# Kernel optimization log

Measured on AMD Instinct MI355X. Metric: run time of the kernel, lower is better.

## Reference

```python
import jax, jax.numpy as jnp
import numpy as np

S, IN, OUT = 2048, 512, 512
H, KV = 16, 4            # query heads, kv heads (cross-broadcast + averaged)
DQ = DK = DV = 64        # per-head embedding dims


def setup_inputs() -> dict:
    key = jax.random.key(0)
    ks = jax.random.split(key, 5)
    lim_in = 1.0 / np.sqrt(IN)
    lim_o = 1.0 / np.sqrt(H * DV)
    x = jax.random.normal(ks[0], (S, IN), dtype=jnp.float32)
    Wq = jax.random.uniform(ks[1], (H * DQ, IN), jnp.float32, -lim_in, lim_in)
    Wk = jax.random.uniform(ks[2], (KV * DK, IN), jnp.float32, -lim_in, lim_in)
    Wv = jax.random.uniform(ks[3], (KV * DV, IN), jnp.float32, -lim_in, lim_in)
    Wo = jax.random.uniform(ks[4], (OUT, H * DV), jnp.float32, -lim_o, lim_o)
    return {"x": x, "Wq": Wq, "Wk": Wk, "Wv": Wv, "Wo": Wo}


def reference(x, Wq, Wk, Wv, Wo):
    seq = x.shape[0]
    # projections (eqx.nn.Linear: y = W @ x, no bias)
    q = (x @ Wq.T).reshape(seq, H, DQ)    # [S, H, DQ]
    k = (x @ Wk.T).reshape(seq, KV, DK)   # [S, KV, DK]
    v = (x @ Wv.T).reshape(seq, KV, DV)   # [S, KV, DV]
    # cross-broadcast every kv head against every query head -> [KV, H, S, S]
    scores = jnp.einsum('shd,tkd->khst', q, k) / jnp.sqrt(jnp.asarray(DK, x.dtype))
    # NOTE: original applies causal mask whenever `mask is not None`; the
    # boolean flag is always passed, so masking is effectively always on.
    causal = jnp.tril(jnp.ones((seq, seq), dtype=bool))
    scores = jnp.where(causal, scores, -jnp.inf)
    w = jax.nn.softmax(scores, axis=-1)   # [KV, H, S, S]
    # attn @ V, then sum over kv heads and average by KV
    o = jnp.einsum('khst,tkd->shd', w, v) / KV  # [S, H, DV]
    return o.reshape(seq, H * DV) @ Wo.T        # [S, OUT]
```

## Files before the change

kernel.cpp:

```cpp
#include <hip/hip_runtime.h>
#include <hip/hip_bf16.h>

#define SEQ   2048
#define INF_  512
#define HQ    16
#define KVH   4
#define DH    64
#define NQ    (HQ*DH)
#define NKV   (KVH*DH)
#define OUTD  512

typedef short v8s __attribute__((ext_vector_type(8)));
typedef float v4f __attribute__((ext_vector_type(4)));

static __device__ __forceinline__ float bf2f(unsigned short u) {
    union { unsigned int i; float f; } c;
    c.i = ((unsigned int)u) << 16;
    return c.f;
}
static __device__ __forceinline__ unsigned short f2bf(float f) {
    union { float f; unsigned int i; } c; c.f = f;
    unsigned int lsb = (c.i >> 16) & 1u;
    c.i += 0x7fffu + lsb;
    return (unsigned short)(c.i >> 16);
}
static __device__ __forceinline__ unsigned int f2bf2(float lo, float hi) {
    union { __hip_bfloat162 h; unsigned int u; } c;
    c.h = __float22bfloat162_rn(make_float2(lo, hi));
    return c.u;
}
static __device__ __forceinline__ v8s pack8(v4f a, v4f b) {
    union { v8s s; uint4 u; } c;
    c.u = make_uint4(f2bf2(a[0], a[1]), f2bf2(a[2], a[3]),
                     f2bf2(b[0], b[1]), f2bf2(b[2], b[3]));
    return c.s;
}

static __device__ __forceinline__ void gll16(const void* g, void* l) {
    __builtin_amdgcn_global_load_lds(
        (const __attribute__((address_space(1))) void*)g,
        (__attribute__((address_space(3))) void*)l, 16, 0, 0);
}

static __device__ __forceinline__ void stage_tile(
    const unsigned short* __restrict__ src, int stride, int kb,
    unsigned short* ldsbase, int w, int lane)
{
#pragma unroll
    for (int i = 0; i < 2; i++) {
        const int rl = w * 16 + i * 8 + (lane >> 3);
        const int kc = ((lane & 7) ^ (rl & 7)) * 8;
        gll16(src + (size_t)rl * stride + kb + kc,
              ldsbase + (w * 16 + i * 8) * 64);
    }
}

static __device__ __forceinline__ void stage_tile32(
    const unsigned short* __restrict__ src, int stride, int kb,
    unsigned short* ldsbase, int w, int lane)
{
    const int rl = w * 8 + (lane >> 3);
    const int kc = ((lane & 7) ^ (rl & 7)) * 8;
    gll16(src + (size_t)rl * stride + kb + kc,
          ldsbase + (w * 8) * 64);
}

#define QSCALE 0.180336880f

__global__ __launch_bounds__(256) void cast_all(
    const float* __restrict__ x,  const float* __restrict__ Wq,
    const float* __restrict__ Wk, const float* __restrict__ Wv,
    const float* __restrict__ Wo,
    unsigned short* __restrict__ xb,  unsigned short* __restrict__ Wqb,
    unsigned short* __restrict__ Wkb, unsigned short* __restrict__ Wvb,
    unsigned short* __restrict__ Wob)
{
    size_t i = ((size_t)blockIdx.x * 256 + threadIdx.x) * 8;
    const float* s; unsigned short* d; size_t off;
    if (i < 1048576)      { s = x;  d = xb;  off = i; }
    else if (i < 1572864) { s = Wq; d = Wqb; off = i - 1048576; }
    else if (i < 1703936) { s = Wk; d = Wkb; off = i - 1572864; }
    else if (i < 1835008) { s = Wv; d = Wvb; off = i - 1703936; }
    else                  { s = Wo; d = Wob; off = i - 1835008; }
    float4 a = *(const float4*)(s + off);
    float4 b = *(const float4*)(s + off + 4);
    *(uint4*)(d + off) = make_uint4(f2bf2(a.x, a.y), f2bf2(a.z, a.w),
                                    f2bf2(b.x, b.y), f2bf2(b.z, b.w));
}

__global__ __launch_bounds__(256, 4) void gemm_qkv(
    const unsigned short* __restrict__ xb,
    const unsigned short* __restrict__ Wqb,
    const unsigned short* __restrict__ Wkb,
    const unsigned short* __restrict__ Wvb,
    unsigned short* __restrict__ Qg,
    unsigned short* __restrict__ Kg,
    unsigned short* __restrict__ Vg)
{
    __shared__ unsigned short Asb[2][4096];
    __shared__ unsigned short Bsb[2][4096];

    const int m0 = blockIdx.x * 64;
    const int n0 = blockIdx.y * 64;

    const unsigned short* Bp; int role;
    if (n0 < NQ)            { Bp = Wqb + (size_t)n0 * INF_;              role = 0; }
    else if (n0 < NQ + NKV) { Bp = Wkb + (size_t)(n0 - NQ) * INF_;       role = 1; }
    else                    { Bp = Wvb + (size_t)(n0 - NQ - NKV) * INF_; role = 2; }

    const int tid = threadIdx.x;
    const int w = tid >> 6, lane = tid & 63;
    const int n = lane & 15, quad = lane >> 4;
    const int m7 = n & 7;
    const int r0w = (w & 1) * 32, c0w = (w >> 1) * 32;
    const unsigned short* Ap = xb + (size_t)m0 * INF_;

    v4f acc[2][2];
#pragma unroll
    for (int rt = 0; rt < 2; rt++)
#pragma unroll
        for (int ct = 0; ct < 2; ct++) acc[rt][ct] = (v4f){0.f,0.f,0.f,0.f};

    stage_tile(Ap, INF_, 0, &Asb[0][0], w, lane);
    stage_tile(Bp, INF_, 0, &Bsb[0][0], w, lane);

    for (int kb = 0; kb < INF_; kb += 64) {
        const int buf = (kb >> 6) & 1;
        __syncthreads();
        if (kb + 64 < INF_) {
            stage_tile(Ap, INF_, kb + 64, &Asb[buf ^ 1][0], w, lane);
            stage_tile(Bp, INF_, kb + 64, &Bsb[buf ^ 1][0], w, lane);
        }
#pragma unroll
        for (int kk = 0; kk < 2; kk++) {
            const int gs = ((kk * 4 + quad) ^ m7) * 8;
            v8s a0 = *(const v8s*)&Asb[buf][(r0w + n) * 64 + gs];
            v8s a1 = *(const v8s*)&Asb[buf][(r0w + 16 + n) * 64 + gs];
            v8s b0 = *(const v8s*)&Bsb[buf][(c0w + n) * 64 + gs];
            v8s b1 = *(const v8s*)&Bsb[buf][(c0w + 16 + n) * 64 + gs];
            acc[0][0] = __builtin_amdgcn_mfma_f32_16x16x32_bf16(a0, b0, acc[0][0], 0, 0, 0);
            acc[0][1] = __builtin_amdgcn_mfma_f32_16x16x32_bf16(a0, b1, acc[0][1], 0, 0, 0);
            acc[1][0] = __builtin_amdgcn_mfma_f32_16x16x32_bf16(a1, b0, acc[1][0], 0, 0, 0);
            acc[1][1] = __builtin_amdgcn_mfma_f32_16x16x32_bf16(a1, b1, acc[1][1], 0, 0, 0);
        }
    }

    const int t = m0 >> 6;
    if (role == 0) {
        unsigned short* base = Qg + ((size_t)(t * 16 + (n0 >> 6))) * 4096;
#pragma unroll
        for (int rt = 0; rt < 2; rt++)
#pragma unroll
            for (int ct = 0; ct < 2; ct++)
#pragma unroll
                for (int reg = 0; reg < 4; reg++) {
                    const int r = r0w + rt * 16 + quad * 4 + reg;
                    const int d = c0w + ct * 16 + n;
                    base[r * 64 + (((d >> 3) ^ (r & 7)) * 8) + (d & 7)] =
                        f2bf(acc[rt][ct][reg] * QSCALE);
                }
    } else if (role == 1) {
        const int g = (n0 - NQ) >> 6;
        unsigned short* base = Kg + ((size_t)(g * 32 + t)) * 4096;
#pragma unroll
        for (int rt = 0; rt < 2; rt++)
#pragma unroll
            for (int ct = 0; ct < 2; ct++)
#pragma unroll
                for (int reg = 0; reg < 4; reg++) {
                    const int r = r0w + rt * 16 + quad * 4 + reg;
                    const int d = c0w + ct * 16 + n;
                    base[r * 64 + (((d >> 3) ^ (r & 7)) * 8) + (d & 7)] =
                        f2bf(acc[rt][ct][reg]);
                }
    } else {
        const int g = (n0 - NQ - NKV) >> 6;
        unsigned short* base = Vg + ((size_t)(g * 32 + t)) * 4096;
#pragma unroll
        for (int rt = 0; rt < 2; rt++)
#pragma unroll
            for (int ct = 0; ct < 2; ct++) {
                const int jb_ = r0w + rt * 16 + quad * 4;
                const int d = c0w + ct * 16 + n;
                const int p = (jb_ & 32) + (((jb_ >> 2) & 3) * 8) + (((jb_ >> 4) & 1) * 4);
                *(uint2*)&base[d * 64 + (((p >> 3) ^ (d & 7)) * 8) + (p & 7)] =
                    make_uint2(f2bf2(acc[rt][ct][0], acc[rt][ct][1]),
                               f2bf2(acc[rt][ct][2], acc[rt][ct][3]));
            }
    }
}

__global__ __launch_bounds__(256, 4) void attn_mfma(
    const unsigned short* __restrict__ Qg,
    const unsigned short* __restrict__ Kg,
    const unsigned short* __restrict__ Vg,
    unsigned short* __restrict__ Oh)
{
    __shared__ unsigned short Ksb[2][4096];
    __shared__ unsigned short Vsb[2][4096];

    const int bx = blockIdx.x;
    const int h  = bx & 15;
    const int p  = (bx >> 4) & 7;
    const int g  = bx >> 7;
    const int tid = threadIdx.x;
    const int w = tid >> 6, lane = tid & 63;
    const int n = lane & 15, quad = lane >> 4;
    const int r0 = w * 32;
    const int m7 = n & 7;

    v8s ones;
#pragma unroll
    for (int i = 0; i < 8; i++) ones[i] = (short)0x3F80;
    const v4f z = (v4f){0.f,0.f,0.f,0.f};

    unsigned short* Ohp = Oh + (size_t)g * ((size_t)SEQ * NQ);

    for (int half = 0; half < 2; half++) {
        const int qi2 = half ? (15 - p) : p;
        const int q0  = qi2 * 128;
        const int ntile = 2 * qi2 + 2;

        {
            const size_t off = ((size_t)(g * 32)) * 4096 + w * 1024 + lane * 8;
            gll16(Kg + off,       &Ksb[0][w * 1024]);
            gll16(Kg + off + 512, &Ksb[0][w * 1024 + 512]);
            gll16(Vg + off,       &Vsb[0][w * 1024]);
            gll16(Vg + off + 512, &Vsb[0][w * 1024 + 512]);
        }

        v8s qf[2][2];
        {
            const unsigned short* tb =
                Qg + ((size_t)((2 * qi2 + (r0 >> 6)) * 16 + h)) * 4096 + (r0 & 63) * 64;
#pragma unroll
            for (int qt = 0; qt < 2; qt++) {
                const unsigned short* rp = tb + (qt * 16 + n) * 64;
                qf[qt][0] = *(const v8s*)(rp + (quad ^ m7) * 8);
                qf[qt][1] = *(const v8s*)(rp + ((quad + 4) ^ m7) * 8);
            }
        }

        v4f Lacc[2];
        Lacc[0] = (v4f){0.f,0.f,0.f,0.f};
        Lacc[1] = (v4f){0.f,0.f,0.f,0.f};
        v4f Oacc[2][4];
#pragma unroll
        for (int qt = 0; qt < 2; qt++)
#pragma unroll
            for (int dt = 0; dt < 4; dt++) Oacc[qt][dt] = (v4f){0.f,0.f,0.f,0.f};

        for (int tt = 0; tt < ntile; tt++) {
            const int buf = tt & 1;
            __syncthreads();
            if (tt + 1 < ntile) {
                const size_t off = ((size_t)(g * 32 + tt + 1)) * 4096 + w * 1024 + lane * 8;
                const int nb = buf ^ 1;
                gll16(Kg + off,       &Ksb[nb][w * 1024]);
                gll16(Kg + off + 512, &Ksb[nb][w * 1024 + 512]);
                gll16(Vg + off,       &Vsb[nb][w * 1024]);
                gll16(Vg + off + 512, &Vsb[nb][w * 1024 + 512]);
            }
            const int t0 = tt * 64;
            const bool do0 = (t0 <= q0 + r0 + 15);
            const bool do1 = (t0 <= q0 + r0 + 31);
            if (!do1) continue;

            const unsigned short* Kb = Ksb[buf];
            const unsigned short* Vb = Vsb[buf];

            v4f sc[2][4];
            __builtin_amdgcn_s_setprio(1);
#pragma unroll
            for (int jt = 0; jt < 4; jt++) {
                const int kr = (jt * 16 + n) * 64;
                v8s kf0 = *(const v8s*)&Kb[kr + (quad ^ m7) * 8];
                v8s kf1 = *(const v8s*)&Kb[kr + ((quad + 4) ^ m7) * 8];
                if (do0) {
                    v4f tq = __builtin_amdgcn_mfma_f32_16x16x32_bf16(kf0, qf[0][0], z, 0, 0, 0);
                    sc[0][jt] = __builtin_amdgcn_mfma_f32_16x16x32_bf16(kf1, qf[0][1], tq, 0, 0, 0);
                }
                v4f t1 = __builtin_amdgcn_mfma_f32_16x16x32_bf16(kf0, qf[1][0], z, 0, 0, 0);
                sc[1][jt] = __builtin_amdgcn_mfma_f32_16x16x32_bf16(kf1, qf[1][1], t1, 0, 0, 0);
            }
            __builtin_amdgcn_s_setprio(0);

#pragma unroll
            for (int qt = 0; qt < 2; qt++) {
                if (qt == 0 && !do0) continue;
                const int qg = q0 + r0 + qt * 16 + n;
                if (t0 + 63 > q0 + r0 + qt * 16) {
#pragma unroll
                    for (int jt = 0; jt < 4; jt++) {
                        const int jg = t0 + jt * 16 + quad * 4;
#pragma unroll
                        for (int reg = 0; reg < 4; reg++)
                            sc[qt][jt][reg] = (jg + reg <= qg) ? sc[qt][jt][reg] : -INFINITY;
                    }
                }
#pragma unroll
                for (int jt = 0; jt < 4; jt++)
#pragma unroll
                    for (int reg = 0; reg < 4; reg++)
                        sc[qt][jt][reg] = __builtin_amdgcn_exp2f(sc[qt][jt][reg]);
            }

            v8s pf[2][2];
            if (do0) {
                pf[0][0] = pack8(sc[0][0], sc[0][1]);
                pf[0][1] = pack8(sc[0][2], sc[0][3]);
            }
            pf[1][0] = pack8(sc[1][0], sc[1][1]);
            pf[1][1] = pack8(sc[1][2], sc[1][3]);

            __builtin_amdgcn_s_setprio(1);
            if (do0) {
                Lacc[0] = __builtin_amdgcn_mfma_f32_16x16x32_bf16(ones, pf[0][0], Lacc[0], 0, 0, 0);
                Lacc[0] = __builtin_amdgcn_mfma_f32_16x16x32_bf16(ones, pf[0][1], Lacc[0], 0, 0, 0);
            }
            Lacc[1] = __builtin_amdgcn_mfma_f32_16x16x32_bf16(ones, pf[1][0], Lacc[1], 0, 0, 0);
            Lacc[1] = __builtin_amdgcn_mfma_f32_16x16x32_bf16(ones, pf[1][1], Lacc[1], 0, 0, 0);

#pragma unroll
            for (int dt = 0; dt < 4; dt++) {
                const int vr = (dt * 16 + n) * 64;
                v8s vf0 = *(const v8s*)&Vb[vr + (quad ^ m7) * 8];
                v8s vf1 = *(const v8s*)&Vb[vr + ((quad + 4) ^ m7) * 8];
                if (do0) {
                    Oacc[0][dt] = __builtin_amdgcn_mfma_f32_16x16x32_bf16(vf0, pf[0][0], Oacc[0][dt], 0, 0, 0);
                    Oacc[0][dt] = __builtin_amdgcn_mfma_f32_16x16x32_bf16(vf1, pf[0][1], Oacc[0][dt], 0, 0, 0);
                }
                Oacc[1][dt] = __builtin_amdgcn_mfma_f32_16x16x32_bf16(vf0, pf[1][0], Oacc[1][dt], 0, 0, 0);
                Oacc[1][dt] = __builtin_amdgcn_mfma_f32_16x16x32_bf16(vf1, pf[1][1], Oacc[1][dt], 0, 0, 0);
            }
            __builtin_amdgcn_s_setprio(0);
        }

#pragma unroll
        for (int qt = 0; qt < 2; qt++) {
            const float inv = 0.25f / Lacc[qt][0];
            const int row = q0 + r0 + qt * 16 + n;
            unsigned short* dst = Ohp + (size_t)row * NQ + h * DH + quad * 4;
#pragma unroll
            for (int dt = 0; dt < 4; dt++) {
                uint2 pk = make_uint2(f2bf2(Oacc[qt][dt][0] * inv, Oacc[qt][dt][1] * inv),
                                      f2bf2(Oacc[qt][dt][2] * inv, Oacc[qt][dt][3] * inv));
                *(uint2*)(dst + dt * 16) = pk;
            }
        }
    }
}

__global__ __launch_bounds__(256) void sum4(
    const unsigned short* __restrict__ Oh,
    unsigned short* __restrict__ Os)
{
    const size_t i = ((size_t)blockIdx.x * 256 + threadIdx.x) * 8;
    const size_t plane = (size_t)SEQ * NQ;
    uint4 u0 = *(const uint4*)(Oh + i);
    uint4 u1 = *(const uint4*)(Oh + plane + i);
    uint4 u2 = *(const uint4*)(Oh + 2 * plane + i);
    uint4 u3 = *(const uint4*)(Oh + 3 * plane + i);
    unsigned int ow[4];
#pragma unroll
    for (int q = 0; q < 4; q++) {
        const unsigned int a = ((const unsigned int*)&u0)[q];
        const unsigned int b = ((const unsigned int*)&u1)[q];
        const unsigned int c = ((const unsigned int*)&u2)[q];
        const unsigned int d = ((const unsigned int*)&u3)[q];
        float lo = bf2f((unsigned short)(a & 0xffffu)) + bf2f((unsigned short)(b & 0xffffu))
                 + bf2f((unsigned short)(c & 0xffffu)) + bf2f((unsigned short)(d & 0xffffu));
        float hi = bf2f((unsigned short)(a >> 16)) + bf2f((unsigned short)(b >> 16))
                 + bf2f((unsigned short)(c >> 16)) + bf2f((unsigned short)(d >> 16));
        ow[q] = f2bf2(lo, hi);
    }
    *(uint4*)(Os + i) = make_uint4(ow[0], ow[1], ow[2], ow[3]);
}

__global__ __launch_bounds__(256, 4) void gemm_out(
    const unsigned short* __restrict__ Os,
    const unsigned short* __restrict__ Wob,
    float* __restrict__ C)
{
    __shared__ unsigned short Asb[2][2048];
    __shared__ unsigned short Bsb[2][4096];

    const int m0 = blockIdx.x * 32;
    const int n0 = blockIdx.y * 64;
    const int tid = threadIdx.x;
    const int w = tid >> 6, lane = tid & 63;
    const int n = lane & 15, quad = lane >> 4;
    const int m7 = n & 7;
    const int rw = (w & 1) * 16, cw = (w >> 1) * 32;

    const unsigned short* Ap = Os + (size_t)m0 * NQ;
    const unsigned short* Bp = Wob + (size_t)n0 * NQ;

    v4f acc[2];
    acc[0] = (v4f){0.f,0.f,0.f,0.f};
    acc[1] = (v4f){0.f,0.f,0.f,0.f};

    stage_tile32(Ap, NQ, 0, &Asb[0][0], w, lane);
    stage_tile  (Bp, NQ, 0, &Bsb[0][0], w, lane);

    for (int kb = 0; kb < NQ; kb += 64) {
        const int buf = (kb >> 6) & 1;
        __syncthreads();
        if (kb + 64 < NQ) {
            stage_tile32(Ap, NQ, kb + 64, &Asb[buf ^ 1][0], w, lane);
            stage_tile  (Bp, NQ, kb + 64, &Bsb[buf ^ 1][0], w, lane);
        }
#pragma unroll
        for (int kk = 0; kk < 2; kk++) {
            const int gs = ((kk * 4 + quad) ^ m7) * 8;
            v8s a  = *(const v8s*)&Asb[buf][(rw + n) * 64 + gs];
            v8s b0 = *(const v8s*)&Bsb[buf][(cw + n) * 64 + gs];
            v8s b1 = *(const v8s*)&Bsb[buf][(cw + 16 + n) * 64 + gs];
            acc[0] = __builtin_amdgcn_mfma_f32_16x16x32_bf16(a, b0, acc[0], 0, 0, 0);
            acc[1] = __builtin_amdgcn_mfma_f32_16x16x32_bf16(a, b1, acc[1], 0, 0, 0);
        }
    }

#pragma unroll
    for (int ct = 0; ct < 2; ct++)
#pragma unroll
        for (int reg = 0; reg < 4; reg++) {
            const int row = m0 + rw + quad * 4 + reg;
            const int col = n0 + cw + ct * 16 + n;
            C[(size_t)row * OUTD + col] = acc[ct][reg];
        }
}

extern "C" void kernel_launch(void* const* d_in, const int* in_sizes, int n_in,
                              void* d_out, int out_size, void* d_ws, size_t ws_size,
                              hipStream_t stream) {
    const float* x  = (const float*)d_in[0];
    const float* Wq = (const float*)d_in[1];
    const float* Wk = (const float*)d_in[2];
    const float* Wv = (const float*)d_in[3];
    const float* Wo = (const float*)d_in[4];
    float* out = (float*)d_out;

    char* base = (char*)d_ws;
    unsigned short* Oh  = (unsigned short*)(base);
    unsigned short* xb  = (unsigned short*)(base);
    unsigned short* Wqb = (unsigned short*)(base + 2097152);
    unsigned short* Wkb = (unsigned short*)(base + 3145728);
    unsigned short* Wvb = (unsigned short*)(base + 3407872);
    unsigned short* Qg  = (unsigned short*)(base + 16777216);
    unsigned short* Kg  = (unsigned short*)(base + 20971520);
    unsigned short* Vg  = (unsigned short*)(base + 22020096);
    unsigned short* Wob = (unsigned short*)(base + 23068672);
    unsigned short* Os  = Qg;

    dim3 blk(256);
    cast_all<<<dim3(1152), blk, 0, stream>>>(x, Wq, Wk, Wv, Wo,
                                             xb, Wqb, Wkb, Wvb, Wob);
    gemm_qkv<<<dim3(SEQ / 64, (NQ + 2 * NKV) / 64), blk, 0, stream>>>(
        xb, Wqb, Wkb, Wvb, Qg, Kg, Vg);
    attn_mfma<<<dim3(512), blk, 0, stream>>>(Qg, Kg, Vg, Oh);
    sum4<<<dim3(1024), blk, 0, stream>>>(Oh, Os);
    gemm_out<<<dim3(SEQ / 32, OUTD / 64), blk, 0, stream>>>(Os, Wob, out);
}
```

Baseline: 144.6 us.

## Split attention query tiles across two blocks with 16 rows per wave

Each attention block now handles a 64-row query sub-tile instead of 128 rows, with each wave owning 16 query rows, and the grid doubles to 1024 blocks. The aim is more parallelism and finer causal work balance across the GPU, plus fewer accumulator registers per thread. In exchange, each K/V tile is loaded into shared memory by twice as many blocks, and per-block loop overhead and synchronisation are amortised over less MFMA work. A barrier is added between halves to protect buffer reuse.

```diff
diff --git a/kernel.cpp b/kernel.cpp
--- a/kernel.cpp
+++ b/kernel.cpp
@@ -202,11 +202,11 @@
     const int bx = blockIdx.x;
     const int h  = bx & 15;
     const int p  = (bx >> 4) & 7;
-    const int g  = bx >> 7;
+    const int sp = (bx >> 7) & 1;
+    const int g  = bx >> 8;
     const int tid = threadIdx.x;
     const int w = tid >> 6, lane = tid & 63;
     const int n = lane & 15, quad = lane >> 4;
-    const int r0 = w * 32;
     const int m7 = n & 7;
 
     v8s ones;
@@ -218,8 +218,11 @@
 
     for (int half = 0; half < 2; half++) {
         const int qi2 = half ? (15 - p) : p;
-        const int q0  = qi2 * 128;
-        const int ntile = 2 * qi2 + 2;
+        const int qbase = qi2 * 128 + sp * 64;
+        const int ext = 2 * qi2 + sp + 1;
+        const int rowbase = qbase + w * 16;
+
+        if (half) __syncthreads();
 
         {
             const size_t off = ((size_t)(g * 32)) * 4096 + w * 1024 + lane * 8;
@@ -229,31 +232,23 @@
             gll16(Vg + off + 512, &Vsb[0][w * 1024 + 512]);
         }
 
-        v8s qf[2][2];
+        v8s qf0, qf1;
         {
-            const unsigned short* tb =
-                Qg + ((size_t)((2 * qi2 + (r0 >> 6)) * 16 + h)) * 4096 + (r0 & 63) * 64;
-#pragma unroll
-            for (int qt = 0; qt < 2; qt++) {
-                const unsigned short* rp = tb + (qt * 16 + n) * 64;
-                qf[qt][0] = *(const v8s*)(rp + (quad ^ m7) * 8);
-                qf[qt][1] = *(const v8s*)(rp + ((quad + 4) ^ m7) * 8);
-            }
-        }
-
-        v4f Lacc[2];
-        Lacc[0] = (v4f){0.f,0.f,0.f,0.f};
-        Lacc[1] = (v4f){0.f,0.f,0.f,0.f};
-        v4f Oacc[2][4];
-#pragma unroll
-        for (int qt = 0; qt < 2; qt++)
-#pragma unroll
-            for (int dt = 0; dt < 4; dt++) Oacc[qt][dt] = (v4f){0.f,0.f,0.f,0.f};
-
-        for (int tt = 0; tt < ntile; tt++) {
+            const unsigned short* rp =
+                Qg + ((size_t)((2 * qi2 + sp) * 16 + h)) * 4096 + (w * 16 + n) * 64;
+            qf0 = *(const v8s*)(rp + (quad ^ m7) * 8);
+            qf1 = *(const v8s*)(rp + ((quad + 4) ^ m7) * 8);
+        }
+
+        v4f Lacc = (v4f){0.f,0.f,0.f,0.f};
+        v4f Oacc[4];
+#pragma unroll
+        for (int dt = 0; dt < 4; dt++) Oacc[dt] = (v4f){0.f,0.f,0.f,0.f};
+
+        for (int tt = 0; tt < ext; tt++) {
             const int buf = tt & 1;
             __syncthreads();
-            if (tt + 1 < ntile) {
+            if (tt + 1 < ext) {
                 const size_t off = ((size_t)(g * 32 + tt + 1)) * 4096 + w * 1024 + lane * 8;
                 const int nb = buf ^ 1;
                 gll16(Kg + off,       &Ksb[nb][w * 1024]);
@@ -262,89 +257,63 @@
                 gll16(Vg + off + 512, &Vsb[nb][w * 1024 + 512]);
             }
             const int t0 = tt * 64;
-            const bool do0 = (t0 <= q0 + r0 + 15);
-            const bool do1 = (t0 <= q0 + r0 + 31);
-            if (!do1) continue;
-
             const unsigned short* Kb = Ksb[buf];
             const unsigned short* Vb = Vsb[buf];
 
-            v4f sc[2][4];
+            v4f sc[4];
             __builtin_amdgcn_s_setprio(1);
 #pragma unroll
             for (int jt = 0; jt < 4; jt++) {
                 const int kr = (jt * 16 + n) * 64;
                 v8s kf0 = *(const v8s*)&Kb[kr + (quad ^ m7) * 8];
                 v8s kf1 = *(const v8s*)&Kb[kr + ((quad + 4) ^ m7) * 8];
-                if (do0) {
-                    v4f tq = __builtin_amdgcn_mfma_f32_16x16x32_bf16(kf0, qf[0][0], z, 0, 0, 0);
-                    sc[0][jt] = __builtin_amdgcn_mfma_f32_16x16x32_bf16(kf1, qf[0][1], tq, 0, 0, 0);
+                v4f tq = __builtin_amdgcn_mfma_f32_16x16x32_bf16(kf0, qf0, z, 0, 0, 0);
+                sc[jt] = __builtin_amdgcn_mfma_f32_16x16x32_bf16(kf1, qf1, tq, 0, 0, 0);
+            }
+            __builtin_amdgcn_s_setprio(0);
+
+            if (t0 + 63 > rowbase) {
+                const int qg = rowbase + n;
+#pragma unroll
+                for (int jt = 0; jt < 4; jt++) {
+                    const int jg = t0 + jt * 16 + quad * 4;
+#pragma unroll
+                    for (int reg = 0; reg < 4; reg++)
+                        sc[jt][reg] = (jg + reg <= qg) ? sc[jt][reg] : -INFINITY;
                 }
-                v4f t1 = __builtin_amdgcn_mfma_f32_16x16x32_bf16(kf0, qf[1][0], z, 0, 0, 0);
-                sc[1][jt] = __builtin_amdgcn_mfma_f32_16x16x32_bf16(kf1, qf[1][1], t1, 0, 0, 0);
-            }
-            __builtin_amdgcn_s_setprio(0);
-
-#pragma unroll
-            for (int qt = 0; qt < 2; qt++) {
-                if (qt == 0 && !do0) continue;
-                const int qg = q0 + r0 + qt * 16 + n;
-                if (t0 + 63 > q0 + r0 + qt * 16) {
-#pragma unroll
-                    for (int jt = 0; jt < 4; jt++) {
-                        const int jg = t0 + jt * 16 + quad * 4;
-#pragma unroll
-                        for (int reg = 0; reg < 4; reg++)
-                            sc[qt][jt][reg] = (jg + reg <= qg) ? sc[qt][jt][reg] : -INFINITY;
-                    }
-                }
-#pragma unroll
-                for (int jt = 0; jt < 4; jt++)
-#pragma unroll
-                    for (int reg = 0; reg < 4; reg++)
-                        sc[qt][jt][reg] = __builtin_amdgcn_exp2f(sc[qt][jt][reg]);
-            }
-
-            v8s pf[2][2];
-            if (do0) {
-                pf[0][0] = pack8(sc[0][0], sc[0][1]);
-                pf[0][1] = pack8(sc[0][2], sc[0][3]);
-            }
-            pf[1][0] = pack8(sc[1][0], sc[1][1]);
-            pf[1][1] = pack8(sc[1][2], sc[1][3]);
+            }
+#pragma unroll
+            for (int jt = 0; jt < 4; jt++)
+#pragma unroll
+                for (int reg = 0; reg < 4; reg++)
+                    sc[jt][reg] = __builtin_amdgcn_exp2f(sc[jt][reg]);
+
+            v8s pf0 = pack8(sc[0], sc[1]);
+            v8s pf1 = pack8(sc[2], sc[3]);
 
             __builtin_amdgcn_s_setprio(1);
-            if (do0) {
-                Lacc[0] = __builtin_amdgcn_mfma_f32_16x16x32_bf16(ones, pf[0][0], Lacc[0], 0, 0, 0);
-                Lacc[0] = __builtin_amdgcn_mfma_f32_16x16x32_bf16(ones, pf[0][1], Lacc[0], 0, 0, 0);
-            }
-            Lacc[1] = __builtin_amdgcn_mfma_f32_16x16x32_bf16(ones, pf[1][0], Lacc[1], 0, 0, 0);
-            Lacc[1] = __builtin_amdgcn_mfma_f32_16x16x32_bf16(ones, pf[1][1], Lacc[1], 0, 0, 0);
+            Lacc = __builtin_amdgcn_mfma_f32_16x16x32_bf16(ones, pf0, Lacc, 0, 0, 0);
+            Lacc = __builtin_amdgcn_mfma_f32_16x16x32_bf16(ones, pf1, Lacc, 0, 0, 0);
 
 #pragma unroll
             for (int dt = 0; dt < 4; dt++) {
                 const int vr = (dt * 16 + n) * 64;
                 v8s vf0 = *(const v8s*)&Vb[vr + (quad ^ m7) * 8];
                 v8s vf1 = *(const v8s*)&Vb[vr + ((quad + 4) ^ m7) * 8];
-                if (do0) {
-                    Oacc[0][dt] = __builtin_amdgcn_mfma_f32_16x16x32_bf16(vf0, pf[0][0], Oacc[0][dt], 0, 0, 0);
-                    Oacc[0][dt] = __builtin_amdgcn_mfma_f32_16x16x32_bf16(vf1, pf[0][1], Oacc[0][dt], 0, 0, 0);
-                }
-                Oacc[1][dt] = __builtin_amdgcn_mfma_f32_16x16x32_bf16(vf0, pf[1][0], Oacc[1][dt], 0, 0, 0);
-                Oacc[1][dt] = __builtin_amdgcn_mfma_f32_16x16x32_bf16(vf1, pf[1][1], Oacc[1][dt], 0, 0, 0);
+                Oacc[dt] = __builtin_amdgcn_mfma_f32_16x16x32_bf16(vf0, pf0, Oacc[dt], 0, 0, 0);
+                Oacc[dt] = __builtin_amdgcn_mfma_f32_16x16x32_bf16(vf1, pf1, Oacc[dt], 0, 0, 0);
             }
             __builtin_amdgcn_s_setprio(0);
         }
 
-#pragma unroll
-        for (int qt = 0; qt < 2; qt++) {
-            const float inv = 0.25f / Lacc[qt][0];
-            const int row = q0 + r0 + qt * 16 + n;
+        {
+            const float inv = 0.25f / Lacc[0];
+            const int row = rowbase + n;
             unsigned short* dst = Ohp + (size_t)row * NQ + h * DH + quad * 4;
 #pragma unroll
             for (int dt = 0; dt < 4; dt++) {
-                uint2 pk = make_uint2(f2bf2(Oacc[qt][dt][0] * inv, Oacc[qt][dt][1] * inv),
-                                      f2bf2(Oacc[qt][dt][2] * inv, Oacc[qt][dt][3] * inv));
+                uint2 pk = make_uint2(f2bf2(Oacc[dt][0] * inv, Oacc[dt][1] * inv),
+                                      f2bf2(Oacc[dt][2] * inv, Oacc[dt][3] * inv));
                 *(uint2*)(dst + dt * 16) = pk;
             }
         }
@@ -458,7 +427,7 @@
                                              xb, Wqb, Wkb, Wvb, Wob);
     gemm_qkv<<<dim3(SEQ / 64, (NQ + 2 * NKV) / 64), blk, 0, stream>>>(
         xb, Wqb, Wkb, Wvb, Qg, Kg, Vg);
-    attn_mfma<<<dim3(512), blk, 0, stream>>>(Qg, Kg, Vg, Oh);
+    attn_mfma<<<dim3(1024), blk, 0, stream>>>(Qg, Kg, Vg, Oh);
     sum4<<<dim3(1024), blk, 0, stream>>>(Oh, Os);
     gemm_out<<<dim3(SEQ / 32, OUTD / 64), blk, 0, stream>>>(Os, Wob, out);
 }
```

Result: no change. 142.7 us (-1.3%).
